# Performance work log

Hardware: AMD Instinct MI355X
Metric: run time of the kernel (lower is better)

## Reference

```python
import jax, jax.numpy as jnp
import numpy as np

HEADS = 12
ROT_DIM = 16  # hidden_dim // num_heads // 4
MAX_FREQ = 256
EPS = 1e-5


def _groupnorm(x, w, b, groups, eps=EPS):
    # x: [B, C, H, W, D]; normalize per (group, H, W, D)
    B, C = x.shape[0], x.shape[1]
    xr = x.reshape(B, groups, -1)
    mu = xr.mean(-1, keepdims=True)
    var = xr.var(-1, keepdims=True)
    xn = ((xr - mu) * jax.lax.rsqrt(var + eps)).reshape(x.shape)
    return xn * w.reshape(1, C, 1, 1, 1) + b.reshape(1, C, 1, 1, 1)


def _layernorm(t, w, b, eps=EPS):
    mu = t.mean(-1, keepdims=True)
    var = t.var(-1, keepdims=True)
    return (t - mu) * jax.lax.rsqrt(var + eps) * w + b


def _rotate_half(t):
    # pairs adjacent elements: (x1, x2) -> (-x2, x1)
    x1 = t[..., 0::2]
    x2 = t[..., 1::2]
    return jnp.stack([-x2, x1], axis=-1).reshape(t.shape)


def _axial_freqs(H, W, D, dim=ROT_DIM, max_freq=MAX_FREQ):
    # 'pixel' rotary: base freqs = linspace(1, max_freq/2, dim//2) * pi, pos in [-1, 1]
    base = jnp.linspace(1.0, max_freq / 2.0, dim // 2) * jnp.pi

    def ax(n):
        pos = jnp.linspace(-1.0, 1.0, n)
        f = pos[:, None] * base[None, :]          # [n, dim//2]
        return jnp.repeat(f, 2, axis=-1)           # [n, dim]

    fh = jnp.broadcast_to(ax(H)[:, None, None, :], (H, W, D, dim))
    fw = jnp.broadcast_to(ax(W)[None, :, None, :], (H, W, D, dim))
    fd = jnp.broadcast_to(ax(D)[None, None, :, :], (H, W, D, dim))
    return jnp.concatenate([fh, fw, fd], -1)       # [H, W, D, 3*dim]


def _rope(freqs, t):
    # t: [B, he, H, W, D, hd]; rotate first rot dims, pass rest through
    rot = freqs.shape[-1]
    tl, tr = t[..., :rot], t[..., rot:]
    tl = tl * jnp.cos(freqs) + _rotate_half(tl) * jnp.sin(freqs)
    return jnp.concatenate([tl, tr], -1)


def setup_inputs() -> dict:
    key = jax.random.key(0)
    ks = jax.random.split(key, 14)
    B, C, H, W, D = 2, 768, 16, 16, 8
    hd = C // HEADS
    f32 = jnp.float32
    inp = {
        "x": jax.random.normal(ks[0], (B, C, H, W, D), f32),
        "norm1_w": 1.0 + 0.1 * jax.random.normal(ks[1], (C,), f32),
        "norm1_b": 0.1 * jax.random.normal(ks[2], (C,), f32),
        "gamma_att": 0.01 * jnp.ones((C,), f32),
        "W_fused": jax.random.normal(ks[3], (C, 7 * C), f32) / np.sqrt(C),
        "b_fused": 0.01 * jax.random.normal(ks[4], (7 * C,), f32),
        "qn_w": 1.0 + 0.1 * jax.random.normal(ks[5], (hd,), f32),
        "qn_b": 0.1 * jax.random.normal(ks[6], (hd,), f32),
        "kn_w": 1.0 + 0.1 * jax.random.normal(ks[7], (hd,), f32),
        "kn_b": 0.1 * jax.random.normal(ks[8], (hd,), f32),
        "W_attn": jax.random.normal(ks[9], (C, C), f32) / np.sqrt(C),
        "W_ffout": jax.random.normal(ks[10], (2 * C, C), f32) / np.sqrt(2 * C),
        "b_ffout": 0.01 * jax.random.normal(ks[11], (C,), f32),
        "bcs": 0,
        "axis_order": 0,
    }
    return inp


def reference(x, norm1_w, norm1_b, gamma_att, W_fused, b_fused, qn_w, qn_b,
              kn_w, kn_b, W_attn, W_ffout, b_ffout, bcs, axis_order):
    B, C, H, W, D = x.shape
    he = HEADS
    hd = C // he
    x_in = x

    # GroupNorm over channels (num_groups = num_heads)
    xn = _groupnorm(x, norm1_w, norm1_b, he)
    t = jnp.transpose(xn, (0, 2, 3, 4, 1))             # b h w d c

    fused = t @ W_fused + b_fused                      # b h w d 7C
    ff, q, k, v = jnp.split(fused, [4 * C, 5 * C, 6 * C], axis=-1)

    def to_heads(z):
        return z.reshape(B, H, W, D, he, hd).transpose(0, 4, 1, 2, 3, 5)  # b he h w d c

    q, k, v = to_heads(q), to_heads(k), to_heads(v)
    q = _layernorm(q, qn_w, qn_b)
    k = _layernorm(k, kn_w, kn_b)

    freqs = _axial_freqs(H, W, D)                      # [H, W, D, 48]
    q = _rope(freqs, q)
    k = _rope(freqs, k)

    S = H * W * D
    qf = q.reshape(B, he, S, hd)
    kf = k.reshape(B, he, S, hd)
    vf = v.reshape(B, he, S, hd)

    scale = 1.0 / np.sqrt(hd)
    scores = jnp.einsum('bhqc,bhkc->bhqk', qf, kf) * scale
    attn = jax.nn.softmax(scores, axis=-1)
    out = jnp.einsum('bhqk,bhkc->bhqc', attn, vf)      # b he S hd

    att = out.reshape(B, he, H, W, D, hd).transpose(0, 2, 3, 4, 1, 5).reshape(B, H, W, D, C)
    att_out = att @ W_attn

    # SwiGLU: first half is value, second half gates
    xh, gate = jnp.split(ff, 2, axis=-1)
    ff_out = (jax.nn.silu(gate) * xh) @ W_ffout + b_ffout

    y = gamma_att * (att_out + ff_out)                 # b h w d c
    return jnp.transpose(y, (0, 4, 1, 2, 3)) + x_in    # b c h w d
```

## Files before the change

### kernel.cpp

```cpp
#include <hip/hip_runtime.h>
#include <hip/hip_bf16.h>

#define HE   12
#define HD   64
#define Cc   768
#define C2   1536
#define C4   3072
#define N7   5376
#define Bb   2
#define Ss   2048
#define BSr  4096
#define PI_F 3.14159265358979f

using f32x4  = __attribute__((ext_vector_type(4))) float;
using short8 = __attribute__((ext_vector_type(8))) short;

__device__ __forceinline__ unsigned short f2b(float f) {
    union { float f; unsigned int u; } v; v.f = f;
    unsigned int u = v.u;
    unsigned int r = (u + 0x7fffu + ((u >> 16) & 1u)) >> 16;
    return (unsigned short)r;
}
__device__ __forceinline__ unsigned short f2bt(float f) {
    union { float f; unsigned int u; } v; v.f = f;
    return (unsigned short)(v.u >> 16);
}
__device__ __forceinline__ float b2f(unsigned short s) {
    union { unsigned int u; float f; } v; v.u = ((unsigned int)s) << 16;
    return v.f;
}
__device__ __forceinline__ f32x4 mfma16(short8 a, short8 b, f32x4 c) {
    return __builtin_amdgcn_mfma_f32_16x16x32_bf16(a, b, c, 0, 0, 0);
}
__device__ __forceinline__ void gl_lds16(const unsigned short* g, unsigned short* l) {
    __builtin_amdgcn_global_load_lds(
        (const __attribute__((address_space(1))) unsigned int*)(const void*)g,
        (__attribute__((address_space(3))) unsigned int*)(void*)l, 16, 0, 0);
}

union U8 { uint4 v; unsigned short u[8]; };

__global__ __launch_bounds__(256) void transpose_w(const float* __restrict__ src,
                                                   unsigned short* __restrict__ dst,
                                                   int R, int Ccol) {
    __shared__ float tile[32][33];
    int tx = threadIdx.x & 31, ty = threadIdx.x >> 5;
    int rt = blockIdx.y * 32, ct = blockIdx.x * 32;
#pragma unroll
    for (int i = 0; i < 4; ++i)
        tile[ty + i * 8][tx] = src[(size_t)(rt + ty + i * 8) * Ccol + ct + tx];
    __syncthreads();
#pragma unroll
    for (int i = 0; i < 4; ++i)
        dst[(size_t)(ct + ty + i * 8) * R + rt + tx] = f2b(tile[tx][ty + i * 8]);
}

__global__ __launch_bounds__(256) void gn_stats(const float* __restrict__ x,
                                                float* __restrict__ stat) {
    int j = blockIdx.x;
    const float4* p = (const float4*)(x + (size_t)j * 131072);
    float s = 0.f, ss = 0.f;
    for (int i = threadIdx.x; i < 32768; i += 256) {
        float4 v = p[i];
        s  += v.x + v.y + v.z + v.w;
        ss += v.x * v.x + v.y * v.y + v.z * v.z + v.w * v.w;
    }
#pragma unroll
    for (int m = 1; m < 64; m <<= 1) { s += __shfl_xor(s, m); ss += __shfl_xor(ss, m); }
    __shared__ float ls[4], lss[4];
    int wid = threadIdx.x >> 6;
    if ((threadIdx.x & 63) == 0) { ls[wid] = s; lss[wid] = ss; }
    __syncthreads();
    if (threadIdx.x == 0) {
        s = ls[0] + ls[1] + ls[2] + ls[3];
        ss = lss[0] + lss[1] + lss[2] + lss[3];
        float mu  = s / 131072.0f;
        float var = ss / 131072.0f - mu * mu;
        stat[j * 2]     = mu;
        stat[j * 2 + 1] = rsqrtf(var + 1e-5f);
    }
}

__global__ __launch_bounds__(256) void norm_transpose(const float* __restrict__ x,
                                                      const float* __restrict__ stat,
                                                      const float* __restrict__ w,
                                                      const float* __restrict__ bgn,
                                                      unsigned short* __restrict__ t) {
    __shared__ float tile[32][33];
    int b = blockIdx.z;
    int st = blockIdx.x * 32, ct = blockIdx.y * 32;
    int tx = threadIdx.x & 31, ty = threadIdx.x >> 5;
#pragma unroll
    for (int i = 0; i < 4; ++i) {
        int c = ct + ty + i * 8;
        int g = c >> 6;
        float mu = stat[(b * 12 + g) * 2], rs = stat[(b * 12 + g) * 2 + 1];
        float v = x[(size_t)(b * Cc + c) * Ss + st + tx];
        tile[ty + i * 8][tx] = (v - mu) * rs * w[c] + bgn[c];
    }
    __syncthreads();
#pragma unroll
    for (int i = 0; i < 4; ++i) {
        int s = st + ty + i * 8, c = ct + tx;
        t[(size_t)(b * Ss + s) * Cc + c] = f2b(tile[tx][ty + i * 8]);
    }
}

template<bool ACCUM, bool BIAS, bool OUTBF16>
__global__ __launch_bounds__(256) void gemm128(const unsigned short* __restrict__ A,
                                               const unsigned short* __restrict__ Bt,
                                               const float* __restrict__ bias,
                                               void* __restrict__ Cout,
                                               int M, int N, int K) {
    __shared__ __align__(16) unsigned short As[128 * 32];
    __shared__ __align__(16) unsigned short Bs[128 * 32];
    const int tid = threadIdx.x;
    const int wid = tid >> 6, lane = tid & 63;
    const int lr = lane & 15, lh = lane >> 4;
    const int wr = wid >> 1, wc = wid & 1;
    const int row0 = blockIdx.y * 128, col0 = blockIdx.x * 128;
    const unsigned short* ga = A  + (size_t)(row0 + (tid >> 2)) * K + (tid & 3) * 8;
    const unsigned short* gb = Bt + (size_t)(col0 + (tid >> 2)) * K + (tid & 3) * 8;
    f32x4 acc[4][4] = {};

    for (int k0 = 0; k0 < K; k0 += 32) {
        gl_lds16(ga + k0,          &As[tid * 8]);
        gl_lds16(ga + 64 * K + k0, &As[2048 + tid * 8]);
        gl_lds16(gb + k0,          &Bs[tid * 8]);
        gl_lds16(gb + 64 * K + k0, &Bs[2048 + tid * 8]);
        __syncthreads();
        short8 af[4], bfr[4];
#pragma unroll
        for (int m = 0; m < 4; ++m) af[m]  = *(const short8*)&As[(wr * 64 + m * 16 + lr) * 32 + lh * 8];
#pragma unroll
        for (int n = 0; n < 4; ++n) bfr[n] = *(const short8*)&Bs[(wc * 64 + n * 16 + lr) * 32 + lh * 8];
#pragma unroll
        for (int m = 0; m < 4; ++m)
#pragma unroll
            for (int n = 0; n < 4; ++n)
                acc[m][n] = mfma16(af[m], bfr[n], acc[m][n]);
        __syncthreads();
    }

#pragma unroll
    for (int m = 0; m < 4; ++m)
#pragma unroll
        for (int n = 0; n < 4; ++n) {
            int row = row0 + wr * 64 + m * 16 + lh * 4;
            int col = col0 + wc * 64 + n * 16 + lr;
            float bv = BIAS ? bias[col] : 0.0f;
#pragma unroll
            for (int r = 0; r < 4; ++r) {
                size_t idx = (size_t)(row + r) * N + col;
                float v = acc[m][n][r] + bv;
                if (ACCUM) v += ((const float*)Cout)[idx];
                if (OUTBF16) ((unsigned short*)Cout)[idx] = f2b(v);
                else         ((float*)Cout)[idx] = v;
            }
        }
}

__global__ __launch_bounds__(256) void qkv_prep(const unsigned short* __restrict__ fused,
                                                const float* __restrict__ qnw, const float* __restrict__ qnb,
                                                const float* __restrict__ knw, const float* __restrict__ knb,
                                                unsigned short* __restrict__ qf,
                                                unsigned short* __restrict__ kf,
                                                unsigned short* __restrict__ vf) {
    const int wid = threadIdx.x >> 6, lane = threadIdx.x & 63;
    const int job = blockIdx.x * 4 + wid;
    const int srow = job / 12, h = job % 12;
    const int b = srow >> 11, s = srow & 2047;

    size_t base = (size_t)srow * N7 + C4 + h * HD;
    float qv = b2f(fused[base + lane]);
    float kv = b2f(fused[base + Cc + lane]);
    float vv = b2f(fused[base + 2 * Cc + lane]);

    float qs = qv, ks = kv;
#pragma unroll
    for (int m = 1; m < 64; m <<= 1) { qs += __shfl_xor(qs, m); ks += __shfl_xor(ks, m); }
    float qmu = qs * (1.0f / 64.0f), kmu = ks * (1.0f / 64.0f);
    float qd = qv - qmu, kd = kv - kmu;
    float qv2 = qd * qd, kv2 = kd * kd;
#pragma unroll
    for (int m = 1; m < 64; m <<= 1) { qv2 += __shfl_xor(qv2, m); kv2 += __shfl_xor(kv2, m); }
    float qn = qd * rsqrtf(qv2 * (1.0f / 64.0f) + 1e-5f) * qnw[lane] + qnb[lane];
    float kn = kd * rsqrtf(kv2 * (1.0f / 64.0f) + 1e-5f) * knw[lane] + knb[lane];

    if (lane < 48) {
        int axis = lane >> 4, ii = (lane & 15) >> 1;
        float basef = (1.0f + (float)ii * (127.0f / 7.0f)) * PI_F;
        int   pos_i = (axis == 0) ? (s >> 7) : (axis == 1) ? ((s >> 3) & 15) : (s & 7);
        float denom = (axis == 2) ? 7.0f : 15.0f;
        float pos   = -1.0f + 2.0f * (float)pos_i / denom;
        float ang   = pos * basef;
        float sn, cs;
        sincosf(ang, &sn, &cs);
        float qp = __shfl_xor(qn, 1);
        float kp = __shfl_xor(kn, 1);
        qn = (lane & 1) ? (qn * cs + qp * sn) : (qn * cs - qp * sn);
        kn = (lane & 1) ? (kn * cs + kp * sn) : (kn * cs - kp * sn);
    }

    size_t obase = ((size_t)(b * 12 + h) * Ss + s) * HD + lane;
    qf[obase] = f2b(qn);
    kf[obase] = f2b(kn);
    vf[obase] = f2b(vv);
}

__global__ __launch_bounds__(256) void ffa_prep(const unsigned short* __restrict__ fused,
                                                unsigned short* __restrict__ ffa) {
    int i8 = blockIdx.x * 256 + threadIdx.x;
    int row = i8 / 192, co = (i8 % 192) * 8;
    U8 xa, ga, oa;
    xa.v = *(const uint4*)&fused[(size_t)row * N7 + co];
    ga.v = *(const uint4*)&fused[(size_t)row * N7 + C2 + co];
#pragma unroll
    for (int j = 0; j < 8; ++j) {
        float g = b2f(ga.u[j]);
        float xh = b2f(xa.u[j]);
        float sg = 1.0f / (1.0f + __expf(-g));
        oa.u[j] = f2b(g * sg * xh);
    }
    *(uint4*)&ffa[(size_t)row * C2 + co] = oa.v;
}

__global__ __launch_bounds__(256) void attn64(const unsigned short* __restrict__ qf,
                                              const unsigned short* __restrict__ kf,
                                              const unsigned short* __restrict__ vf,
                                              unsigned short* __restrict__ att) {
    __shared__ __align__(16) unsigned short Ks[64][80];
    __shared__ __align__(16) unsigned short Vt[64][80];
    __shared__ __align__(16) unsigned short Ps[4][16][80];
    const int tid = threadIdx.x, wid = tid >> 6, lane = tid & 63;
    const int lr = lane & 15, lh = lane >> 4;
    const int bh = blockIdx.y, qt = blockIdx.x;
    const int b = bh / 12, h = bh % 12;
    const size_t kvbase = (size_t)bh * Ss * HD;

    const int qrow = qt * 64 + wid * 16 + lr;
    short8 qa0 = *(const short8*)&qf[kvbase + (size_t)qrow * HD + lh * 8];
    short8 qa1 = *(const short8*)&qf[kvbase + (size_t)qrow * HD + 32 + lh * 8];

    const int r0 = tid >> 3, kc0 = (tid & 7) * 8;
    const int sv0 = (((r0 >> 3) ^ (kc0 >> 3)) << 3) | (r0 & 7);
    const int sv1 = ((((r0 >> 3) + 4) ^ (kc0 >> 3)) << 3) | (r0 & 7);
    const unsigned short* kptr = kf + kvbase + (size_t)r0 * HD + kc0;
    const unsigned short* vptr = vf + kvbase + (size_t)r0 * HD + kc0;

    const short8 ones = {0x3F80, 0x3F80, 0x3F80, 0x3F80, 0x3F80, 0x3F80, 0x3F80, 0x3F80};
    const float c1 = 0.125f * 1.44269504f;
    const float c2 = 23.08312065f;
    const int rxb = (lr >> 2) & 3;

    f32x4 oacc[4] = {};
    f32x4 lacc = {};

    uint4 kreg0 = *(const uint4*)kptr;
    uint4 kreg1 = *(const uint4*)(kptr + 32 * HD);
    U8 vreg0, vreg1;
    vreg0.v = *(const uint4*)vptr;
    vreg1.v = *(const uint4*)(vptr + 32 * HD);

    for (int kt = 0; kt < 32; ++kt) {
        *(uint4*)&Ks[r0][kc0]      = kreg0;
        *(uint4*)&Ks[r0 + 32][kc0] = kreg1;
#pragma unroll
        for (int j = 0; j < 8; ++j) Vt[kc0 + j][sv0] = vreg0.u[j];
#pragma unroll
        for (int j = 0; j < 8; ++j) Vt[kc0 + j][sv1] = vreg1.u[j];
        __syncthreads();

        if (kt < 31) {
            const unsigned short* kp = kptr + (size_t)(kt + 1) * 64 * HD;
            const unsigned short* vp = vptr + (size_t)(kt + 1) * 64 * HD;
            kreg0 = *(const uint4*)kp;
            kreg1 = *(const uint4*)(kp + 32 * HD);
            vreg0.v = *(const uint4*)vp;
            vreg1.v = *(const uint4*)(vp + 32 * HD);
        }

        f32x4 sc[4];
#pragma unroll
        for (int n = 0; n < 4; ++n) {
            f32x4 z = {0.f, 0.f, 0.f, 0.f};
            short8 k0 = *(const short8*)&Ks[n * 16 + lr][lh * 8];
            short8 k1 = *(const short8*)&Ks[n * 16 + lr][32 + lh * 8];
            z = mfma16(qa0, k0, z);
            z = mfma16(qa1, k1, z);
            sc[n] = z;
        }

#pragma unroll
        for (int n = 0; n < 4; ++n)
#pragma unroll
            for (int r = 0; r < 4; ++r)
                sc[n][r] = exp2f(sc[n][r] * c1 - c2);

#pragma unroll
        for (int r = 0; r < 4; ++r) {
            int prow = lh * 4 + r;
            int lo = lr & 7, lr3 = lr >> 3;
            Ps[wid][prow][(((0 + lr3) ^ lh) << 3) | lo] = f2bt(sc[0][r]);
            Ps[wid][prow][(((2 + lr3) ^ lh) << 3) | lo] = f2bt(sc[1][r]);
            Ps[wid][prow][(((4 + lr3) ^ lh) << 3) | lo] = f2bt(sc[2][r]);
            Ps[wid][prow][(((6 + lr3) ^ lh) << 3) | lo] = f2bt(sc[3][r]);
        }

        short8 pa0 = *(const short8*)&Ps[wid][lr][((lh ^ rxb) & 7) * 8];
        short8 pa1 = *(const short8*)&Ps[wid][lr][(((lh + 4) ^ rxb) & 7) * 8];
        lacc = mfma16(pa0, ones, lacc);
        lacc = mfma16(pa1, ones, lacc);
#pragma unroll
        for (int n = 0; n < 4; ++n) {
            int dv = (2 * n + (lr >> 3)) & 7;
            short8 v0 = *(const short8*)&Vt[n * 16 + lr][((lh ^ dv) & 7) * 8];
            short8 v1 = *(const short8*)&Vt[n * 16 + lr][(((lh + 4) ^ dv) & 7) * 8];
            oacc[n] = mfma16(pa0, v0, oacc[n]);
            oacc[n] = mfma16(pa1, v1, oacc[n]);
        }
        __syncthreads();
    }

#pragma unroll
    for (int n = 0; n < 4; ++n)
#pragma unroll
        for (int r = 0; r < 4; ++r) {
            int srow_w = qt * 64 + wid * 16 + lh * 4 + r;
            int col = h * HD + n * 16 + lr;
            att[(size_t)(b * Ss + srow_w) * Cc + col] = f2b(oacc[n][r] / lacc[r]);
        }
}

__global__ __launch_bounds__(256) void final_out(const float* __restrict__ oacc,
                                                 const float* __restrict__ x,
                                                 const float* __restrict__ gamma,
                                                 float* __restrict__ out) {
    __shared__ float tile[32][33];
    int b = blockIdx.z;
    int st = blockIdx.x * 32, ct = blockIdx.y * 32;
    int tx = threadIdx.x & 31, ty = threadIdx.x >> 5;
#pragma unroll
    for (int i = 0; i < 4; ++i) {
        int s = st + ty + i * 8;
        tile[ty + i * 8][tx] = oacc[(size_t)(b * Ss + s) * Cc + ct + tx];
    }
    __syncthreads();
#pragma unroll
    for (int i = 0; i < 4; ++i) {
        int c = ct + ty + i * 8;
        size_t idx = (size_t)(b * Cc + c) * Ss + st + tx;
        out[idx] = gamma[c] * tile[tx][ty + i * 8] + x[idx];
    }
}

extern "C" void kernel_launch(void* const* d_in, const int* in_sizes, int n_in,
                              void* d_out, int out_size, void* d_ws, size_t ws_size,
                              hipStream_t stream) {
    const float* x     = (const float*)d_in[0];
    const float* n1w   = (const float*)d_in[1];
    const float* n1b   = (const float*)d_in[2];
    const float* gamma = (const float*)d_in[3];
    const float* Wf    = (const float*)d_in[4];
    const float* bfu   = (const float*)d_in[5];
    const float* qnw   = (const float*)d_in[6];
    const float* qnb   = (const float*)d_in[7];
    const float* knw   = (const float*)d_in[8];
    const float* knb   = (const float*)d_in[9];
    const float* Wa    = (const float*)d_in[10];
    const float* Wo    = (const float*)d_in[11];
    const float* bo    = (const float*)d_in[12];

    char* ws = (char*)d_ws;
    size_t off = 0;
    auto alloc = [&](size_t bytes) {
        char* p = ws + off;
        off = (off + bytes + 255) & ~(size_t)255;
        return p;
    };
    float*          stat  = (float*)alloc(24 * 2 * 4);
    unsigned short* t     = (unsigned short*)alloc((size_t)BSr * Cc * 2);
    unsigned short* WtF   = (unsigned short*)alloc((size_t)N7 * Cc * 2);
    unsigned short* fused = (unsigned short*)alloc((size_t)BSr * N7 * 2);
    unsigned short* qfB   = (unsigned short*)alloc((size_t)Bb * HE * Ss * HD * 2);
    unsigned short* kfB   = (unsigned short*)alloc((size_t)Bb * HE * Ss * HD * 2);
    unsigned short* vfB   = (unsigned short*)alloc((size_t)Bb * HE * Ss * HD * 2);
    unsigned short* ffa   = (unsigned short*)alloc((size_t)BSr * C2 * 2);
    unsigned short* WtA   = (unsigned short*)alloc((size_t)Cc * Cc * 2);
    unsigned short* WtO   = (unsigned short*)alloc((size_t)Cc * C2 * 2);
    unsigned short* attB  = t;
    float*          oacc  = (float*)fused;

    transpose_w<<<dim3(N7 / 32, Cc / 32), 256, 0, stream>>>(Wf, WtF, Cc, N7);
    transpose_w<<<dim3(Cc / 32, Cc / 32), 256, 0, stream>>>(Wa, WtA, Cc, Cc);
    transpose_w<<<dim3(Cc / 32, C2 / 32), 256, 0, stream>>>(Wo, WtO, C2, Cc);

    gn_stats<<<24, 256, 0, stream>>>(x, stat);
    norm_transpose<<<dim3(Ss / 32, Cc / 32, Bb), 256, 0, stream>>>(x, stat, n1w, n1b, t);

    gemm128<false, true, true><<<dim3(N7 / 128, BSr / 128), 256, 0, stream>>>(
        t, WtF, bfu, fused, BSr, N7, Cc);

    qkv_prep<<<(Bb * Ss * HE) / 4, 256, 0, stream>>>(fused, qnw, qnb, knw, knb, qfB, kfB, vfB);
    ffa_prep<<<(BSr * C2 / 8) / 256, 256, 0, stream>>>(fused, ffa);

    attn64<<<dim3(Ss / 64, Bb * HE), 256, 0, stream>>>(qfB, kfB, vfB, attB);

    gemm128<false, false, false><<<dim3(Cc / 128, BSr / 128), 256, 0, stream>>>(
        attB, WtA, nullptr, oacc, BSr, Cc, Cc);
    gemm128<true, true, false><<<dim3(Cc / 128, BSr / 128), 256, 0, stream>>>(
        ffa, WtO, bo, oacc, BSr, Cc, C2);

    final_out<<<dim3(Ss / 32, Cc / 32, Bb), 256, 0, stream>>>(oacc, x, gamma, (float*)d_out);
}
```

Measured before the change: 387.9 us.

## Fuse final epilogue into FFN GEMM, swizzle GEMM tiles per XCD, double-buffer attention

```diff
diff --git a/kernel.cpp b/kernel.cpp
--- a/kernel.cpp
+++ b/kernel.cpp
@@ -36,6 +36,13 @@
     __builtin_amdgcn_global_load_lds(
         (const __attribute__((address_space(1))) unsigned int*)(const void*)g,
         (__attribute__((address_space(3))) unsigned int*)(void*)l, 16, 0, 0);
+}
+__device__ __forceinline__ void xcd_tile(int& bx, int& by) {
+    int nx = gridDim.x;
+    int flat = blockIdx.y * nx + blockIdx.x;
+    int nwg = nx * gridDim.y;
+    int swz = (flat & 7) * (nwg >> 3) + (flat >> 3);
+    bx = swz % nx; by = swz / nx;
 }
 
 union U8 { uint4 v; unsigned short u[8]; };
@@ -118,7 +125,8 @@
     const int wid = tid >> 6, lane = tid & 63;
     const int lr = lane & 15, lh = lane >> 4;
     const int wr = wid >> 1, wc = wid & 1;
-    const int row0 = blockIdx.y * 128, col0 = blockIdx.x * 128;
+    int bx, by; xcd_tile(bx, by);
+    const int row0 = by * 128, col0 = bx * 128;
     const unsigned short* ga = A  + (size_t)(row0 + (tid >> 2)) * K + (tid & 3) * 8;
     const unsigned short* gb = Bt + (size_t)(col0 + (tid >> 2)) * K + (tid & 3) * 8;
     f32x4 acc[4][4] = {};
@@ -156,6 +164,63 @@
                 if (ACCUM) v += ((const float*)Cout)[idx];
                 if (OUTBF16) ((unsigned short*)Cout)[idx] = f2b(v);
                 else         ((float*)Cout)[idx] = v;
+            }
+        }
+}
+
+__global__ __launch_bounds__(256) void gemm_fin(const unsigned short* __restrict__ A,
+                                                const unsigned short* __restrict__ Bt,
+                                                const float* __restrict__ bo,
+                                                const float* __restrict__ oaccIn,
+                                                const float* __restrict__ x,
+                                                const float* __restrict__ gamma,
+                                                float* __restrict__ out,
+                                                int M, int N, int K) {
+    __shared__ __align__(16) unsigned short As[128 * 32];
+    __shared__ __align__(16) unsigned short Bs[128 * 32];
+    const int tid = threadIdx.x;
+    const int wid = tid >> 6, lane = tid & 63;
+    const int lr = lane & 15, lh = lane >> 4;
+    const int wr = wid >> 1, wc = wid & 1;
+    int bx, by; xcd_tile(bx, by);
+    const int row0 = by * 128, col0 = bx * 128;
+    const unsigned short* ga = A  + (size_t)(row0 + (tid >> 2)) * K + (tid & 3) * 8;
+    const unsigned short* gb = Bt + (size_t)(col0 + (tid >> 2)) * K + (tid & 3) * 8;
+    f32x4 acc[4][4] = {};
+
+    for (int k0 = 0; k0 < K; k0 += 32) {
+        gl_lds16(ga + k0,          &As[tid * 8]);
+        gl_lds16(ga + 64 * K + k0, &As[2048 + tid * 8]);
+        gl_lds16(gb + k0,          &Bs[tid * 8]);
+        gl_lds16(gb + 64 * K + k0, &Bs[2048 + tid * 8]);
+        __syncthreads();
+        short8 af[4], bfr[4];
+#pragma unroll
+        for (int m = 0; m < 4; ++m) af[m]  = *(const short8*)&As[(wr * 64 + m * 16 + lr) * 32 + lh * 8];
+#pragma unroll
+        for (int n = 0; n < 4; ++n) bfr[n] = *(const short8*)&Bs[(wc * 64 + n * 16 + lr) * 32 + lh * 8];
+#pragma unroll
+        for (int m = 0; m < 4; ++m)
+#pragma unroll
+            for (int n = 0; n < 4; ++n)
+                acc[m][n] = mfma16(af[m], bfr[n], acc[m][n]);
+        __syncthreads();
+    }
+
+#pragma unroll
+    for (int m = 0; m < 4; ++m)
+#pragma unroll
+        for (int n = 0; n < 4; ++n) {
+            int row = row0 + wr * 64 + m * 16 + lh * 4;
+            int col = col0 + wc * 64 + n * 16 + lr;
+            float bv = bo[col], gv = gamma[col];
+#pragma unroll
+            for (int r = 0; r < 4; ++r) {
+                int rw = row + r;
+                float v = acc[m][n][r] + bv + oaccIn[(size_t)rw * N + col];
+                int b = rw >> 11, s = rw & 2047;
+                size_t oidx = (size_t)(b * Cc + col) * Ss + s;
+                out[oidx] = gv * v + x[oidx];
             }
         }
 }
@@ -229,8 +294,8 @@
                                               const unsigned short* __restrict__ kf,
                                               const unsigned short* __restrict__ vf,
                                               unsigned short* __restrict__ att) {
-    __shared__ __align__(16) unsigned short Ks[64][80];
-    __shared__ __align__(16) unsigned short Vt[64][80];
+    __shared__ __align__(16) unsigned short Ks[2][64][80];
+    __shared__ __align__(16) unsigned short Vt[2][64][80];
     __shared__ __align__(16) unsigned short Ps[4][16][80];
     const int tid = threadIdx.x, wid = tid >> 6, lane = tid & 63;
     const int lr = lane & 15, lh = lane >> 4;
@@ -261,21 +326,34 @@
     U8 vreg0, vreg1;
     vreg0.v = *(const uint4*)vptr;
     vreg1.v = *(const uint4*)(vptr + 32 * HD);
-
+    *(uint4*)&Ks[0][r0][kc0]      = kreg0;
+    *(uint4*)&Ks[0][r0 + 32][kc0] = kreg1;
+#pragma unroll
+    for (int j = 0; j < 8; ++j) Vt[0][kc0 + j][sv0] = vreg0.u[j];
+#pragma unroll
+    for (int j = 0; j < 8; ++j) Vt[0][kc0 + j][sv1] = vreg1.u[j];
+    kreg0   = *(const uint4*)(kptr + 64 * HD);
+    kreg1   = *(const uint4*)(kptr + 96 * HD);
+    vreg0.v = *(const uint4*)(vptr + 64 * HD);
+    vreg1.v = *(const uint4*)(vptr + 96 * HD);
+    __syncthreads();
+
+#pragma unroll 2
     for (int kt = 0; kt < 32; ++kt) {
-        *(uint4*)&Ks[r0][kc0]      = kreg0;
-        *(uint4*)&Ks[r0 + 32][kc0] = kreg1;
-#pragma unroll
-        for (int j = 0; j < 8; ++j) Vt[kc0 + j][sv0] = vreg0.u[j];
-#pragma unroll
-        for (int j = 0; j < 8; ++j) Vt[kc0 + j][sv1] = vreg1.u[j];
-        __syncthreads();
-
+        const int cur = kt & 1;
         if (kt < 31) {
-            const unsigned short* kp = kptr + (size_t)(kt + 1) * 64 * HD;
-            const unsigned short* vp = vptr + (size_t)(kt + 1) * 64 * HD;
-            kreg0 = *(const uint4*)kp;
-            kreg1 = *(const uint4*)(kp + 32 * HD);
+            *(uint4*)&Ks[cur ^ 1][r0][kc0]      = kreg0;
+            *(uint4*)&Ks[cur ^ 1][r0 + 32][kc0] = kreg1;
+#pragma unroll
+            for (int j = 0; j < 8; ++j) Vt[cur ^ 1][kc0 + j][sv0] = vreg0.u[j];
+#pragma unroll
+            for (int j = 0; j < 8; ++j) Vt[cur ^ 1][kc0 + j][sv1] = vreg1.u[j];
+        }
+        if (kt < 30) {
+            const unsigned short* kp = kptr + (size_t)(kt + 2) * 64 * HD;
+            const unsigned short* vp = vptr + (size_t)(kt + 2) * 64 * HD;
+            kreg0   = *(const uint4*)kp;
+            kreg1   = *(const uint4*)(kp + 32 * HD);
             vreg0.v = *(const uint4*)vp;
             vreg1.v = *(const uint4*)(vp + 32 * HD);
         }
@@ -284,8 +362,8 @@
 #pragma unroll
         for (int n = 0; n < 4; ++n) {
             f32x4 z = {0.f, 0.f, 0.f, 0.f};
-            short8 k0 = *(const short8*)&Ks[n * 16 + lr][lh * 8];
-            short8 k1 = *(const short8*)&Ks[n * 16 + lr][32 + lh * 8];
+            short8 k0 = *(const short8*)&Ks[cur][n * 16 + lr][lh * 8];
+            short8 k1 = *(const short8*)&Ks[cur][n * 16 + lr][32 + lh * 8];
             z = mfma16(qa0, k0, z);
             z = mfma16(qa1, k1, z);
             sc[n] = z;
@@ -314,44 +392,25 @@
 #pragma unroll
         for (int n = 0; n < 4; ++n) {
             int dv = (2 * n + (lr >> 3)) & 7;
-            short8 v0 = *(const short8*)&Vt[n * 16 + lr][((lh ^ dv) & 7) * 8];
-            short8 v1 = *(const short8*)&Vt[n * 16 + lr][(((lh + 4) ^ dv) & 7) * 8];
+            short8 v0 = *(const short8*)&Vt[cur][n * 16 + lr][((lh ^ dv) & 7) * 8];
+            short8 v1 = *(const short8*)&Vt[cur][n * 16 + lr][(((lh + 4) ^ dv) & 7) * 8];
             oacc[n] = mfma16(pa0, v0, oacc[n]);
             oacc[n] = mfma16(pa1, v1, oacc[n]);
         }
         __syncthreads();
     }
 
+    float rinv[4];
+#pragma unroll
+    for (int r = 0; r < 4; ++r) rinv[r] = 1.0f / lacc[r];
 #pragma unroll
     for (int n = 0; n < 4; ++n)
 #pragma unroll
         for (int r = 0; r < 4; ++r) {
             int srow_w = qt * 64 + wid * 16 + lh * 4 + r;
             int col = h * HD + n * 16 + lr;
-            att[(size_t)(b * Ss + srow_w) * Cc + col] = f2b(oacc[n][r] / lacc[r]);
-        }
-}
-
-__global__ __launch_bounds__(256) void final_out(const float* __restrict__ oacc,
-                                                 const float* __restrict__ x,
-                                                 const float* __restrict__ gamma,
-                                                 float* __restrict__ out) {
-    __shared__ float tile[32][33];
-    int b = blockIdx.z;
-    int st = blockIdx.x * 32, ct = blockIdx.y * 32;
-    int tx = threadIdx.x & 31, ty = threadIdx.x >> 5;
-#pragma unroll
-    for (int i = 0; i < 4; ++i) {
-        int s = st + ty + i * 8;
-        tile[ty + i * 8][tx] = oacc[(size_t)(b * Ss + s) * Cc + ct + tx];
-    }
-    __syncthreads();
-#pragma unroll
-    for (int i = 0; i < 4; ++i) {
-        int c = ct + ty + i * 8;
-        size_t idx = (size_t)(b * Cc + c) * Ss + st + tx;
-        out[idx] = gamma[c] * tile[tx][ty + i * 8] + x[idx];
-    }
+            att[(size_t)(b * Ss + srow_w) * Cc + col] = f2b(oacc[n][r] * rinv[r]);
+        }
 }
 
 extern "C" void kernel_launch(void* const* d_in, const int* in_sizes, int n_in,
@@ -408,8 +467,6 @@
 
     gemm128<false, false, false><<<dim3(Cc / 128, BSr / 128), 256, 0, stream>>>(
         attB, WtA, nullptr, oacc, BSr, Cc, Cc);
-    gemm128<true, true, false><<<dim3(Cc / 128, BSr / 128), 256, 0, stream>>>(
-        ffa, WtO, bo, oacc, BSr, Cc, C2);
-
-    final_out<<<dim3(Ss / 32, Cc / 32, Bb), 256, 0, stream>>>(oacc, x, gamma, (float*)d_out);
-}
+    gemm_fin<<<dim3(Cc / 128, BSr / 128), 256, 0, stream>>>(
+        ffa, WtO, bo, oacc, x, gamma, (float*)d_out, BSr, Cc, C2);
+}
```

Result: faster. 370.8 us (-4.4%).
